# Optimization experiments

Hardware: AMD Instinct MI355X
Metric: run time of the kernel (lower is better)

The kernel has to match this reference:

```python
import jax, jax.numpy as jnp
import numpy as np

N = 100000
E = 1600000
IN, HID, OUT = 128, 32, 32


def gcn_conv(x, ei, ew, W, b, n):
    # PyG GCNConv: symmetric norm with self-loops, edge_attr as edge weight
    h = x @ W                                  # [n, d_out]
    row, col = ei[0], ei[1]
    loop = jnp.arange(n)
    row = jnp.concatenate([row, loop])
    col = jnp.concatenate([col, loop])
    ew = jnp.concatenate([ew, jnp.ones((n,), ew.dtype)])
    deg = jax.ops.segment_sum(ew, col, num_segments=n)
    dinv = jnp.where(deg > 0, jax.lax.rsqrt(deg), 0.0)
    norm = dinv[row] * ew * dinv[col]          # [E+n]
    out = jax.ops.segment_sum(norm[:, None] * h[row], col, num_segments=n)
    return out + b


def setup_inputs() -> dict:
    key = jax.random.key(0)
    ks = jax.random.split(key, 24)
    inp = {}
    for i in range(3):
        inp[f"x{i+1}"] = jax.random.normal(ks[i], (N, IN), jnp.float32)
        inp[f"ei{i+1}"] = jax.random.randint(ks[3 + i], (2, E), 0, N, jnp.int64)
        inp[f"ea{i+1}"] = jax.random.uniform(ks[6 + i], (E,), jnp.float32)
        inp[f"W{i+1}"] = jax.random.normal(ks[9 + i], (IN, HID), jnp.float32) * (IN ** -0.5)
        inp[f"b{i+1}"] = jnp.zeros((HID,), jnp.float32)
        inp[f"Wo{i+1}"] = jax.random.normal(ks[12 + i], (HID, OUT), jnp.float32) * (HID ** -0.5)
        inp[f"bo{i+1}"] = jnp.zeros((OUT,), jnp.float32)
    inp["att_w"] = jax.random.normal(ks[15], (HID, 1), jnp.float32) * (HID ** -0.5)
    return inp


def reference(x1, x2, x3, ei1, ei2, ei3, ea1, ea2, ea3,
              W1, W2, W3, b1, b2, b3,
              Wo1, Wo2, Wo3, bo1, bo2, bo3, att_w):
    xs = [x1, x2, x3]
    eis = [ei1, ei2, ei3]
    eas = [ea1, ea2, ea3]
    Ws = [W1, W2, W3]
    bs = [b1, b2, b3]
    Wos = [Wo1, Wo2, Wo3]
    bos = [bo1, bo2, bo3]

    embs, coefs = [], []
    for x, ei, ea, W, b in zip(xs, eis, eas, Ws, bs):
        e = jax.nn.relu(gcn_conv(x, ei, ea, W, b, N))   # [N, HID]; dropout is eval no-op
        embs.append(e)
        coefs.append(jnp.exp(jax.nn.leaky_relu(e @ att_w)))  # [N, 1]
    coef_sum = coefs[0] + coefs[1] + coefs[2]
    weights = [c / coef_sum for c in coefs]
    h = sum(w * e for w, e in zip(weights, embs))       # [N, HID]

    out = sum(gcn_conv(h, ei, ea, Wo, bo, N)
              for ei, ea, Wo, bo in zip(eis, eas, Wos, bos))
    return (out, weights[0], weights[1], weights[2])
```

## Files before the change

### kernel.cpp

```cpp
#include <hip/hip_runtime.h>
#include <hip/hip_fp16.h>

typedef unsigned short u16;
typedef unsigned int   u32;
typedef _Float16 h2 __attribute__((ext_vector_type(2)));

#define N_NODES 100000
#define N_EDGES 1600000
#define IN_DIM  128
#define HID_DIM 32
#define OUT_DIM 32

#define BK   128
#define NBC  782
#define NBT  (3 * NBC)

#define PB    256
#define BINB  1024
#define CHUNK 18750
#define SC_N  (NBT * PB)
#define SC_CHUNK 2048
#define SC_G  ((SC_N + SC_CHUNK - 1) / SC_CHUNK)
#define CAP  3072
#define GN4  ((N_NODES * 4 + 255) / 256)
#define MM2  ((N_NODES + 63) / 64)

#define KEYB 4
#define NKEY (BK << KEYB)

__device__ inline int ofs_at(const int* __restrict__ rp1, const int* __restrict__ bs, int m) {
    return m ? rp1[m] + bs[(m - 1) >> 11] : 0;
}


__global__ void binhist_kernel(const int* __restrict__ ei0, const int* __restrict__ ei1,
                               const int* __restrict__ ei2, int* __restrict__ hist_t) {
    __shared__ int hloc[NBT];
    for (int i = threadIdx.x; i < NBT; i += blockDim.x) hloc[i] = 0;
    __syncthreads();
    int b = blockIdx.x;
    int beg = b * CHUNK, end = beg + CHUNK;
    for (int e = beg + threadIdx.x; e < end; e += blockDim.x) {
        int c = (e >= 2 * N_EDGES) ? 2 : (e >= N_EDGES ? 1 : 0);
        const int* ei = (c == 0) ? ei0 : (c == 1) ? ei1 : ei2;
        int col = ei[N_EDGES + (e - c * N_EDGES)];
        atomicAdd(&hloc[c * NBC + (col >> 7)], 1);
    }
    __syncthreads();
    for (int g = threadIdx.x; g < NBT; g += blockDim.x)
        hist_t[g * PB + b] = hloc[g];
}


__global__ void scan1_kernel(const int* __restrict__ counts, int* __restrict__ rp1,
                             int* __restrict__ blocksum) {
    __shared__ int wsum[4];
    int tid = threadIdx.x;
    int base = blockIdx.x * SC_CHUNK + tid * 8;
    int vals[8];
    int tsum = 0;
    if (base < SC_N) {
        int4 v0 = *(const int4*)(counts + base);
        int4 v1 = *(const int4*)(counts + base + 4);
        vals[0] = v0.x; vals[1] = v0.y; vals[2] = v0.z; vals[3] = v0.w;
        vals[4] = v1.x; vals[5] = v1.y; vals[6] = v1.z; vals[7] = v1.w;
#pragma unroll
        for (int k = 0; k < 8; k++) tsum += vals[k];
    } else {
#pragma unroll
        for (int k = 0; k < 8; k++) vals[k] = 0;
    }
    int lane = tid & 63, wave = tid >> 6;
    int x = tsum;
    for (int d = 1; d < 64; d <<= 1) {
        int t = __shfl_up(x, d, 64);
        if (lane >= d) x += t;
    }
    if (lane == 63) wsum[wave] = x;
    __syncthreads();
    int woff = 0;
    for (int w = 0; w < wave; w++) woff += wsum[w];
    int run = woff + x - tsum;
    if (base < SC_N) {
#pragma unroll
        for (int k = 0; k < 8; k++) {
            run += vals[k];
            rp1[base + k + 1] = run;
        }
    }
    if (tid == blockDim.x - 1) blocksum[blockIdx.x] = woff + x;
    if (blockIdx.x == 0 && tid == 0) rp1[0] = 0;
}

__global__ void scan2_kernel(int* __restrict__ blocksum, int n) {
    __shared__ int wsum[4];
    int tid = threadIdx.x;
    int lane = tid & 63, wave = tid >> 6;
    int carry = 0;
    for (int base = 0; base < n; base += 256) {
        int i = base + tid;
        int v = (i < n) ? blocksum[i] : 0;
        int x = v;
        for (int d = 1; d < 64; d <<= 1) {
            int t = __shfl_up(x, d, 64);
            if (lane >= d) x += t;
        }
        if (lane == 63) wsum[wave] = x;
        __syncthreads();
        int woff = 0;
        for (int w = 0; w < wave; w++) woff += wsum[w];
        int total = wsum[0] + wsum[1] + wsum[2] + wsum[3];
        if (i < n) blocksum[i] = carry + woff + x - v;
        carry += total;
        __syncthreads();
    }
}


__global__ void binscatter_kernel(const int* __restrict__ ei0, const int* __restrict__ ei1,
                                  const int* __restrict__ ei2,
                                  const float* __restrict__ ea0, const float* __restrict__ ea1,
                                  const float* __restrict__ ea2,
                                  const int* __restrict__ rp1, const int* __restrict__ bsum,
                                  int2* __restrict__ stg) {
    __shared__ int base_l[NBT];
    int b = blockIdx.x;
    for (int g = threadIdx.x; g < NBT; g += blockDim.x)
        base_l[g] = ofs_at(rp1, bsum, g * PB + b);
    __syncthreads();
    int beg = b * CHUNK, end = beg + CHUNK;
    for (int e = beg + threadIdx.x; e < end; e += blockDim.x) {
        int c = (e >= 2 * N_EDGES) ? 2 : (e >= N_EDGES ? 1 : 0);
        int le = e - c * N_EDGES;
        const int* ei = (c == 0) ? ei0 : (c == 1) ? ei1 : ei2;
        const float* ea = (c == 0) ? ea0 : (c == 1) ? ea1 : ea2;
        int row = ei[le];
        int col = ei[N_EDGES + le];
        int g = c * NBC + (col >> 7);
        int slot = atomicAdd(&base_l[g], 1);
        stg[slot] = make_int2(row | ((col & 127) << 17), __float_as_int(ea[le]));
    }
}


__global__ void bucket_sort_kernel(const int2* __restrict__ stg, const int* __restrict__ rp1,
                                   const int* __restrict__ bsum,
                                   u32* __restrict__ csr,
                                   float* __restrict__ dinv, int* __restrict__ row_ptr) {
    __shared__ int2 buf[CAP];
    __shared__ int hist[NKEY];
    __shared__ int fill[NKEY];
    __shared__ float deg[BK];
    __shared__ float dl[BK];
    __shared__ int wsum[4];
    int tid = threadIdx.x;
    int g = blockIdx.x;
    int c = g / NBC;
    int colBase = (g % NBC) << 7;
    for (int i = tid; i < NKEY; i += 256) { hist[i] = 0; fill[i] = 0; }
    if (tid < BK) deg[tid] = 1.0f;
    __syncthreads();
    int beg = ofs_at(rp1, bsum, g * PB);
    int end = (g == NBT - 1) ? 3 * N_EDGES : ofs_at(rp1, bsum, (g + 1) * PB);
    int cnt = end - beg;
    if (cnt > CAP) cnt = CAP;
    for (int i = tid; i < cnt; i += blockDim.x) {
        int2 p = stg[beg + i];
        buf[i] = p;
        int cl = (p.x >> 17) & 127;
        int row = p.x & 0x1FFFF;
        atomicAdd(&hist[(cl << KEYB) | (row >> 13)], 1);
        atomicAdd(&deg[cl], __int_as_float(p.y));
    }
    __syncthreads();
    int base8 = tid * 8;
    int v[8]; int tsum = 0;
#pragma unroll
    for (int k = 0; k < 8; k++) { v[k] = hist[base8 + k]; tsum += v[k]; }
    int lane = tid & 63, wave = tid >> 6;
    int xs = tsum;
    for (int d = 1; d < 64; d <<= 1) {
        int tt = __shfl_up(xs, d, 64);
        if (lane >= d) xs += tt;
    }
    if (lane == 63) wsum[wave] = xs;
    __syncthreads();
    int woff = 0;
    for (int w = 0; w < wave; w++) woff += wsum[w];
    int run = woff + xs - tsum;
#pragma unroll
    for (int k = 0; k < 8; k++) { int t2 = v[k]; hist[base8 + k] = run; run += t2; }
    if (tid < BK) dl[tid] = rsqrtf(deg[tid]);
    __syncthreads();
    for (int i = tid; i < cnt; i += blockDim.x) {
        int2 p = buf[i];
        int cl = (p.x >> 17) & 127;
        int row = p.x & 0x1FFFF;
        int key = (cl << KEYB) | (row >> 13);
        int r = atomicAdd(&fill[key], 1);
        float vv = __int_as_float(p.y) * dl[cl];
        __half h = __float2half(vv);
        u32 hb = (u32)(*(u16*)&h) & 0x7FFF;
        csr[beg + hist[key] + r] = (u32)row | (hb << 17);
    }
    int col = colBase + tid;
    if (tid < BK && col < N_NODES) {
        dinv[(size_t)c * N_NODES + col] = dl[tid];
        row_ptr[(size_t)c * N_NODES + col] = beg + hist[tid << KEYB];
    }
    if (g == NBT - 1 && tid == 0) row_ptr[3 * N_NODES] = 3 * N_EDGES;
}


__device__ inline u32 pack_half2(float a, float b) {
    __half2 h = __floats2half2_rn(a, b);
    union { __half2 h; u32 u; } cv; cv.h = h;
    return cv.u;
}

__device__ inline float2 unpack_half2(u32 u) {
    union { u32 u; __half2 h; } cv; cv.u = u;
    return __half22float2(cv.h);
}

__device__ inline float val15(u32 meta) {
    return unpack_half2(meta >> 17).x;
}

__device__ inline float fdot2h(u32 a, u32 b, float c) {
    union { u32 u; h2 h; } ca, cb; ca.u = a; cb.u = b;
    return __builtin_amdgcn_fdot2(ca.h, cb.h, c, false);
}


__global__ void matmul_in3_kernel(const float* __restrict__ x0, const float* __restrict__ x1,
                                  const float* __restrict__ x2,
                                  const float* __restrict__ W0, const float* __restrict__ W1,
                                  const float* __restrict__ W2,
                                  const float* __restrict__ dinv,
                                  u16* __restrict__ h3) {
    __shared__ u32 Ws2[(IN_DIM / 2) * HID_DIM];
    int c = blockIdx.x / MM2;
    int lb = blockIdx.x % MM2;
    const float* x = (c == 0) ? x0 : (c == 1) ? x1 : x2;
    const float* W = (c == 0) ? W0 : (c == 1) ? W1 : W2;
    for (int i = threadIdx.x; i < (IN_DIM / 2) * HID_DIM; i += blockDim.x) {
        int d = i & 31, jp = i >> 5;
        Ws2[i] = pack_half2(W[(2 * jp) * HID_DIM + d], W[(2 * jp + 1) * HID_DIM + d]);
    }
    __syncthreads();
    int t = threadIdx.x & 7;
    int grp = threadIdx.x >> 3;
    int v0 = lb * 64 + grp * 2;
    if (v0 >= N_NODES) return;
    float a[2][4];
#pragma unroll
    for (int k = 0; k < 2; k++)
#pragma unroll
        for (int d = 0; d < 4; d++) a[k][d] = 0.f;
    const float* xr0 = x + (size_t)v0 * IN_DIM;
    const float* xr1 = xr0 + IN_DIM;
#pragma unroll 4
    for (int q = 0; q < 32; q++) {
        float4 xv0 = *(const float4*)(xr0 + 4 * q);
        float4 xv1 = *(const float4*)(xr1 + 4 * q);
        u32 p00 = pack_half2(xv0.x, xv0.y), p01 = pack_half2(xv0.z, xv0.w);
        u32 p10 = pack_half2(xv1.x, xv1.y), p11 = pack_half2(xv1.z, xv1.w);
        uint4 wA = *(const uint4*)&Ws2[(2 * q) * HID_DIM + 4 * t];
        uint4 wB = *(const uint4*)&Ws2[(2 * q + 1) * HID_DIM + 4 * t];
        a[0][0] = fdot2h(p00, wA.x, a[0][0]); a[0][1] = fdot2h(p00, wA.y, a[0][1]);
        a[0][2] = fdot2h(p00, wA.z, a[0][2]); a[0][3] = fdot2h(p00, wA.w, a[0][3]);
        a[0][0] = fdot2h(p01, wB.x, a[0][0]); a[0][1] = fdot2h(p01, wB.y, a[0][1]);
        a[0][2] = fdot2h(p01, wB.z, a[0][2]); a[0][3] = fdot2h(p01, wB.w, a[0][3]);
        a[1][0] = fdot2h(p10, wA.x, a[1][0]); a[1][1] = fdot2h(p10, wA.y, a[1][1]);
        a[1][2] = fdot2h(p10, wA.z, a[1][2]); a[1][3] = fdot2h(p10, wA.w, a[1][3]);
        a[1][0] = fdot2h(p11, wB.x, a[1][0]); a[1][1] = fdot2h(p11, wB.y, a[1][1]);
        a[1][2] = fdot2h(p11, wB.z, a[1][2]); a[1][3] = fdot2h(p11, wB.w, a[1][3]);
    }
#pragma unroll
    for (int k = 0; k < 2; k++) {
        float s = dinv[(size_t)c * N_NODES + v0 + k];
        uint2 pk = make_uint2(pack_half2(a[k][0] * s, a[k][1] * s),
                              pack_half2(a[k][2] * s, a[k][3] * s));
        *(uint2*)(h3 + ((size_t)c * N_NODES + v0 + k) * HID_DIM + 4 * t) = pk;
    }
}


__global__ void matmul_hid3_kernel(const float* __restrict__ hmix,
                                   const float* __restrict__ Wo0, const float* __restrict__ Wo1,
                                   const float* __restrict__ Wo2,
                                   const float* __restrict__ dinv,
                                   u16* __restrict__ h23) {
    __shared__ u32 Ws2[(HID_DIM / 2) * OUT_DIM];
    int c = blockIdx.x / MM2;
    int lb = blockIdx.x % MM2;
    const float* Wo = (c == 0) ? Wo0 : (c == 1) ? Wo1 : Wo2;
    for (int i = threadIdx.x; i < (HID_DIM / 2) * OUT_DIM; i += blockDim.x) {
        int d = i & 31, jp = i >> 5;
        Ws2[i] = pack_half2(Wo[(2 * jp) * OUT_DIM + d], Wo[(2 * jp + 1) * OUT_DIM + d]);
    }
    __syncthreads();
    int t = threadIdx.x & 7;
    int grp = threadIdx.x >> 3;
    int v0 = lb * 64 + grp * 2;
    if (v0 >= N_NODES) return;
    float a[2][4];
#pragma unroll
    for (int k = 0; k < 2; k++)
#pragma unroll
        for (int d = 0; d < 4; d++) a[k][d] = 0.f;
    const float* hr0 = hmix + (size_t)v0 * HID_DIM;
    const float* hr1 = hr0 + HID_DIM;
#pragma unroll
    for (int q = 0; q < 8; q++) {
        float4 xv0 = *(const float4*)(hr0 + 4 * q);
        float4 xv1 = *(const float4*)(hr1 + 4 * q);
        u32 p00 = pack_half2(xv0.x, xv0.y), p01 = pack_half2(xv0.z, xv0.w);
        u32 p10 = pack_half2(xv1.x, xv1.y), p11 = pack_half2(xv1.z, xv1.w);
        uint4 wA = *(const uint4*)&Ws2[(2 * q) * OUT_DIM + 4 * t];
        uint4 wB = *(const uint4*)&Ws2[(2 * q + 1) * OUT_DIM + 4 * t];
        a[0][0] = fdot2h(p00, wA.x, a[0][0]); a[0][1] = fdot2h(p00, wA.y, a[0][1]);
        a[0][2] = fdot2h(p00, wA.z, a[0][2]); a[0][3] = fdot2h(p00, wA.w, a[0][3]);
        a[0][0] = fdot2h(p01, wB.x, a[0][0]); a[0][1] = fdot2h(p01, wB.y, a[0][1]);
        a[0][2] = fdot2h(p01, wB.z, a[0][2]); a[0][3] = fdot2h(p01, wB.w, a[0][3]);
        a[1][0] = fdot2h(p10, wA.x, a[1][0]); a[1][1] = fdot2h(p10, wA.y, a[1][1]);
        a[1][2] = fdot2h(p10, wA.z, a[1][2]); a[1][3] = fdot2h(p10, wA.w, a[1][3]);
        a[1][0] = fdot2h(p11, wB.x, a[1][0]); a[1][1] = fdot2h(p11, wB.y, a[1][1]);
        a[1][2] = fdot2h(p11, wB.z, a[1][2]); a[1][3] = fdot2h(p11, wB.w, a[1][3]);
    }
#pragma unroll
    for (int k = 0; k < 2; k++) {
        float s = dinv[(size_t)c * N_NODES + v0 + k];
        uint2 pk = make_uint2(pack_half2(a[k][0] * s, a[k][1] * s),
                              pack_half2(a[k][2] * s, a[k][3] * s));
        *(uint2*)(h23 + ((size_t)c * N_NODES + v0 + k) * OUT_DIM + 4 * t) = pk;
    }
}


__global__ void gather_combine_kernel(const int* __restrict__ row_ptr,
                                      const u32* __restrict__ csr,
                                      const u16* __restrict__ h3,
                                      const float* __restrict__ dinv,
                                      const float* __restrict__ b0,
                                      const float* __restrict__ b1,
                                      const float* __restrict__ b2,
                                      const float* __restrict__ att_w,
                                      float* __restrict__ hmix,
                                      float* __restrict__ wout) {
    int gid = blockIdx.x * blockDim.x + threadIdx.x;
    int v = gid >> 2;
    int t = gid & 3;
    if (v >= N_NODES) return;
    float4 wv0 = *(const float4*)(att_w + t * 8);
    float4 wv1 = *(const float4*)(att_w + t * 8 + 4);
    float e[3][8];
    float coef[3];
#pragma unroll
    for (int c = 0; c < 3; c++) {
        const u16* h = h3 + (size_t)c * N_NODES * HID_DIM;
        const float* bb = (c == 0) ? b0 : (c == 1) ? b1 : b2;
        int beg = row_ptr[c * N_NODES + v], end = row_ptr[c * N_NODES + v + 1];
        float a[8];
#pragma unroll
        for (int k = 0; k < 8; k++) a[k] = 0.f;
        int ee = beg;
        for (; ee + 4 <= end; ee += 4) {
            u32 m0 = csr[ee], m1 = csr[ee + 1], m2 = csr[ee + 2], m3 = csr[ee + 3];
            uint4 u0 = *(const uint4*)(h + (size_t)(m0 & 0x1FFFF) * HID_DIM + 8 * t);
            uint4 u1 = *(const uint4*)(h + (size_t)(m1 & 0x1FFFF) * HID_DIM + 8 * t);
            uint4 u2 = *(const uint4*)(h + (size_t)(m2 & 0x1FFFF) * HID_DIM + 8 * t);
            uint4 u3 = *(const uint4*)(h + (size_t)(m3 & 0x1FFFF) * HID_DIM + 8 * t);
            float vl0 = val15(m0), vl1 = val15(m1), vl2 = val15(m2), vl3 = val15(m3);
            float2 f;
            f = unpack_half2(u0.x); a[0] += vl0 * f.x; a[1] += vl0 * f.y;
            f = unpack_half2(u0.y); a[2] += vl0 * f.x; a[3] += vl0 * f.y;
            f = unpack_half2(u0.z); a[4] += vl0 * f.x; a[5] += vl0 * f.y;
            f = unpack_half2(u0.w); a[6] += vl0 * f.x; a[7] += vl0 * f.y;
            f = unpack_half2(u1.x); a[0] += vl1 * f.x; a[1] += vl1 * f.y;
            f = unpack_half2(u1.y); a[2] += vl1 * f.x; a[3] += vl1 * f.y;
            f = unpack_half2(u1.z); a[4] += vl1 * f.x; a[5] += vl1 * f.y;
            f = unpack_half2(u1.w); a[6] += vl1 * f.x; a[7] += vl1 * f.y;
            f = unpack_half2(u2.x); a[0] += vl2 * f.x; a[1] += vl2 * f.y;
            f = unpack_half2(u2.y); a[2] += vl2 * f.x; a[3] += vl2 * f.y;
            f = unpack_half2(u2.z); a[4] += vl2 * f.x; a[5] += vl2 * f.y;
            f = unpack_half2(u2.w); a[6] += vl2 * f.x; a[7] += vl2 * f.y;
            f = unpack_half2(u3.x); a[0] += vl3 * f.x; a[1] += vl3 * f.y;
            f = unpack_half2(u3.y); a[2] += vl3 * f.x; a[3] += vl3 * f.y;
            f = unpack_half2(u3.z); a[4] += vl3 * f.x; a[5] += vl3 * f.y;
            f = unpack_half2(u3.w); a[6] += vl3 * f.x; a[7] += vl3 * f.y;
        }
        for (; ee < end; ee++) {
            u32 m = csr[ee];
            float vl = val15(m);
            uint4 u = *(const uint4*)(h + (size_t)(m & 0x1FFFF) * HID_DIM + 8 * t);
            float2 f;
            f = unpack_half2(u.x); a[0] += vl * f.x; a[1] += vl * f.y;
            f = unpack_half2(u.y); a[2] += vl * f.x; a[3] += vl * f.y;
            f = unpack_half2(u.z); a[4] += vl * f.x; a[5] += vl * f.y;
            f = unpack_half2(u.w); a[6] += vl * f.x; a[7] += vl * f.y;
        }
        float s = dinv[(size_t)c * N_NODES + v];
        uint4 u = *(const uint4*)(h + (size_t)v * HID_DIM + 8 * t);
        float2 f0 = unpack_half2(u.x), f1 = unpack_half2(u.y);
        float2 f2 = unpack_half2(u.z), f3 = unpack_half2(u.w);
        float4 bv0 = *(const float4*)(bb + t * 8);
        float4 bv1 = *(const float4*)(bb + t * 8 + 4);
        e[c][0] = fmaxf(a[0] + s * f0.x + bv0.x, 0.f);
        e[c][1] = fmaxf(a[1] + s * f0.y + bv0.y, 0.f);
        e[c][2] = fmaxf(a[2] + s * f1.x + bv0.z, 0.f);
        e[c][3] = fmaxf(a[3] + s * f1.y + bv0.w, 0.f);
        e[c][4] = fmaxf(a[4] + s * f2.x + bv1.x, 0.f);
        e[c][5] = fmaxf(a[5] + s * f2.y + bv1.y, 0.f);
        e[c][6] = fmaxf(a[6] + s * f3.x + bv1.z, 0.f);
        e[c][7] = fmaxf(a[7] + s * f3.y + bv1.w, 0.f);
        float dot = e[c][0] * wv0.x + e[c][1] * wv0.y + e[c][2] * wv0.z + e[c][3] * wv0.w
                  + e[c][4] * wv1.x + e[c][5] * wv1.y + e[c][6] * wv1.z + e[c][7] * wv1.w;
        dot += __shfl_xor(dot, 1, 64);
        dot += __shfl_xor(dot, 2, 64);
        float lr = (dot > 0.0f) ? dot : 0.01f * dot;
        coef[c] = expf(lr);
    }
    float inv = 1.0f / (coef[0] + coef[1] + coef[2]);
    float w0 = coef[0] * inv, w1 = coef[1] * inv, w2 = coef[2] * inv;
    if (t == 0) {
        wout[v] = w0;
        wout[N_NODES + v] = w1;
        wout[2 * N_NODES + v] = w2;
    }
    float4 r0, r1;
    r0.x = w0 * e[0][0] + w1 * e[1][0] + w2 * e[2][0];
    r0.y = w0 * e[0][1] + w1 * e[1][1] + w2 * e[2][1];
    r0.z = w0 * e[0][2] + w1 * e[1][2] + w2 * e[2][2];
    r0.w = w0 * e[0][3] + w1 * e[1][3] + w2 * e[2][3];
    r1.x = w0 * e[0][4] + w1 * e[1][4] + w2 * e[2][4];
    r1.y = w0 * e[0][5] + w1 * e[1][5] + w2 * e[2][5];
    r1.z = w0 * e[0][6] + w1 * e[1][6] + w2 * e[2][6];
    r1.w = w0 * e[0][7] + w1 * e[1][7] + w2 * e[2][7];
    *(float4*)(hmix + (size_t)v * HID_DIM + t * 8) = r0;
    *(float4*)(hmix + (size_t)v * HID_DIM + t * 8 + 4) = r1;
}


__global__ void gather_out_kernel(const int* __restrict__ row_ptr,
                                  const u32* __restrict__ csr,
                                  const u16* __restrict__ h23,
                                  const float* __restrict__ dinv,
                                  const float* __restrict__ bo0,
                                  const float* __restrict__ bo1,
                                  const float* __restrict__ bo2,
                                  float* __restrict__ out) {
    int gid = blockIdx.x * blockDim.x + threadIdx.x;
    int v = gid >> 2;
    int t = gid & 3;
    if (v >= N_NODES) return;
    float4 p0 = *(const float4*)(bo0 + t * 8);
    float4 p1 = *(const float4*)(bo0 + t * 8 + 4);
    float4 q0 = *(const float4*)(bo1 + t * 8);
    float4 q1 = *(const float4*)(bo1 + t * 8 + 4);
    float4 s0 = *(const float4*)(bo2 + t * 8);
    float4 s1 = *(const float4*)(bo2 + t * 8 + 4);
    float a[8];
    a[0] = p0.x + q0.x + s0.x; a[1] = p0.y + q0.y + s0.y;
    a[2] = p0.z + q0.z + s0.z; a[3] = p0.w + q0.w + s0.w;
    a[4] = p1.x + q1.x + s1.x; a[5] = p1.y + q1.y + s1.y;
    a[6] = p1.z + q1.z + s1.z; a[7] = p1.w + q1.w + s1.w;
#pragma unroll
    for (int c = 0; c < 3; c++) {
        const u16* h2m = h23 + (size_t)c * N_NODES * OUT_DIM;
        int beg = row_ptr[c * N_NODES + v], end = row_ptr[c * N_NODES + v + 1];
        int ee = beg;
        for (; ee + 4 <= end; ee += 4) {
            u32 m0 = csr[ee], m1 = csr[ee + 1], m2 = csr[ee + 2], m3 = csr[ee + 3];
            uint4 u0 = *(const uint4*)(h2m + (size_t)(m0 & 0x1FFFF) * OUT_DIM + 8 * t);
            uint4 u1 = *(const uint4*)(h2m + (size_t)(m1 & 0x1FFFF) * OUT_DIM + 8 * t);
            uint4 u2 = *(const uint4*)(h2m + (size_t)(m2 & 0x1FFFF) * OUT_DIM + 8 * t);
            uint4 u3 = *(const uint4*)(h2m + (size_t)(m3 & 0x1FFFF) * OUT_DIM + 8 * t);
            float vl0 = val15(m0), vl1 = val15(m1), vl2 = val15(m2), vl3 = val15(m3);
            float2 f;
            f = unpack_half2(u0.x); a[0] += vl0 * f.x; a[1] += vl0 * f.y;
            f = unpack_half2(u0.y); a[2] += vl0 * f.x; a[3] += vl0 * f.y;
            f = unpack_half2(u0.z); a[4] += vl0 * f.x; a[5] += vl0 * f.y;
            f = unpack_half2(u0.w); a[6] += vl0 * f.x; a[7] += vl0 * f.y;
            f = unpack_half2(u1.x); a[0] += vl1 * f.x; a[1] += vl1 * f.y;
            f = unpack_half2(u1.y); a[2] += vl1 * f.x; a[3] += vl1 * f.y;
            f = unpack_half2(u1.z); a[4] += vl1 * f.x; a[5] += vl1 * f.y;
            f = unpack_half2(u1.w); a[6] += vl1 * f.x; a[7] += vl1 * f.y;
            f = unpack_half2(u2.x); a[0] += vl2 * f.x; a[1] += vl2 * f.y;
            f = unpack_half2(u2.y); a[2] += vl2 * f.x; a[3] += vl2 * f.y;
            f = unpack_half2(u2.z); a[4] += vl2 * f.x; a[5] += vl2 * f.y;
            f = unpack_half2(u2.w); a[6] += vl2 * f.x; a[7] += vl2 * f.y;
            f = unpack_half2(u3.x); a[0] += vl3 * f.x; a[1] += vl3 * f.y;
            f = unpack_half2(u3.y); a[2] += vl3 * f.x; a[3] += vl3 * f.y;
            f = unpack_half2(u3.z); a[4] += vl3 * f.x; a[5] += vl3 * f.y;
            f = unpack_half2(u3.w); a[6] += vl3 * f.x; a[7] += vl3 * f.y;
        }
        for (; ee < end; ee++) {
            u32 m = csr[ee];
            float vl = val15(m);
            uint4 u = *(const uint4*)(h2m + (size_t)(m & 0x1FFFF) * OUT_DIM + 8 * t);
            float2 f;
            f = unpack_half2(u.x); a[0] += vl * f.x; a[1] += vl * f.y;
            f = unpack_half2(u.y); a[2] += vl * f.x; a[3] += vl * f.y;
            f = unpack_half2(u.z); a[4] += vl * f.x; a[5] += vl * f.y;
            f = unpack_half2(u.w); a[6] += vl * f.x; a[7] += vl * f.y;
        }
        float s = dinv[(size_t)c * N_NODES + v];
        uint4 u = *(const uint4*)(h2m + (size_t)v * OUT_DIM + 8 * t);
        float2 f0 = unpack_half2(u.x), f1 = unpack_half2(u.y);
        float2 f2 = unpack_half2(u.z), f3 = unpack_half2(u.w);
        a[0] += s * f0.x; a[1] += s * f0.y; a[2] += s * f1.x; a[3] += s * f1.y;
        a[4] += s * f2.x; a[5] += s * f2.y; a[6] += s * f3.x; a[7] += s * f3.y;
    }
    float4 o0, o1;
    o0.x = a[0]; o0.y = a[1]; o0.z = a[2]; o0.w = a[3];
    o1.x = a[4]; o1.y = a[5]; o1.z = a[6]; o1.w = a[7];
    *(float4*)(out + (size_t)v * OUT_DIM + t * 8) = o0;
    *(float4*)(out + (size_t)v * OUT_DIM + t * 8 + 4) = o1;
}


extern "C" void kernel_launch(void* const* d_in, const int* in_sizes, int n_in,
                              void* d_out, int out_size, void* d_ws, size_t ws_size,
                              hipStream_t stream) {
    const float* x[3];  const int* ei[3];  const float* ea[3];
    const float* W[3];  const float* b[3]; const float* Wo[3]; const float* bo[3];
    for (int c = 0; c < 3; c++) {
        x[c]  = (const float*)d_in[7 * c + 0];
        ei[c] = (const int*)  d_in[7 * c + 1];
        ea[c] = (const float*)d_in[7 * c + 2];
        W[c]  = (const float*)d_in[7 * c + 3];
        b[c]  = (const float*)d_in[7 * c + 4];
        Wo[c] = (const float*)d_in[7 * c + 5];
        bo[c] = (const float*)d_in[7 * c + 6];
    }
    const float* att_w = (const float*)d_in[21];
    float* out = (float*)d_out;
    float* wout = out + (size_t)N_NODES * OUT_DIM;

    int*   wsb      = (int*)d_ws;
    float* dinv     = (float*)wsb;
    int*   row_ptr  = wsb + 3 * N_NODES;
    int*   blocksum = row_ptr + 3 * N_NODES + 4;
    size_t stg_off  = (size_t)(3 * N_NODES + 3 * N_NODES + 4 + 512);
    stg_off = (stg_off + 3) & ~(size_t)3;
    int2*  stg      = (int2*)(wsb + stg_off);
    u32*   csr      = (u32*)(stg + 3 * (size_t)N_EDGES);
    u16*   hA       = (u16*)(csr + 3 * (size_t)N_EDGES);
    int*   hist_t   = (int*)hA;
    int*   rp1      = hist_t + SC_N;
    float* hmix     = (float*)(hA + 3 * (size_t)N_NODES * HID_DIM);

    const int B = 256;

    binhist_kernel<<<PB, BINB, 0, stream>>>(ei[0], ei[1], ei[2], hist_t);
    scan1_kernel<<<SC_G, B, 0, stream>>>(hist_t, rp1, blocksum);
    scan2_kernel<<<1, B, 0, stream>>>(blocksum, SC_G);
    binscatter_kernel<<<PB, BINB, 0, stream>>>(ei[0], ei[1], ei[2], ea[0], ea[1], ea[2],
                                               rp1, blocksum, stg);
    bucket_sort_kernel<<<NBT, B, 0, stream>>>(stg, rp1, blocksum, csr, dinv, row_ptr);

    matmul_in3_kernel<<<3 * MM2, B, 0, stream>>>(x[0], x[1], x[2], W[0], W[1], W[2],
                                                 dinv, hA);
    gather_combine_kernel<<<GN4, B, 0, stream>>>(row_ptr, csr, hA, dinv,
                                                 b[0], b[1], b[2], att_w, hmix, wout);

    matmul_hid3_kernel<<<3 * MM2, B, 0, stream>>>(hmix, Wo[0], Wo[1], Wo[2], dinv, hA);
    gather_out_kernel<<<GN4, B, 0, stream>>>(row_ptr, csr, hA, dinv,
                                             bo[0], bo[1], bo[2], out);
}
```

Before: 576.8 us.

## Widen sort buckets to 512 columns and drop shared-memory edge staging buffer

Each bucket now covers 512 destination columns instead of 128, so there are 4x fewer bucket-sort blocks, each handling about 8k edges. The shared-memory staging buffer and CAP clamp are removed, and the second pass re-reads the staging array from global memory. Fill counters are replaced by atomically incrementing the scanned histogram in place, and column start offsets are saved separately. This lowers block count and removes the overflow truncation, but each block does more serial work, re-reads global memory and holds a larger 32-entry register array per thread for the scan.

```diff
diff --git a/kernel.cpp b/kernel.cpp
--- a/kernel.cpp
+++ b/kernel.cpp
@@ -11,8 +11,8 @@
 #define HID_DIM 32
 #define OUT_DIM 32
 
-#define BK   128
-#define NBC  782
+#define BK   512
+#define NBC  196
 #define NBT  (3 * NBC)
 
 #define PB    256
@@ -21,7 +21,6 @@
 #define SC_N  (NBT * PB)
 #define SC_CHUNK 2048
 #define SC_G  ((SC_N + SC_CHUNK - 1) / SC_CHUNK)
-#define CAP  3072
 #define GN4  ((N_NODES * 4 + 255) / 256)
 #define MM2  ((N_NODES + 63) / 64)
 
@@ -44,7 +43,7 @@
         int c = (e >= 2 * N_EDGES) ? 2 : (e >= N_EDGES ? 1 : 0);
         const int* ei = (c == 0) ? ei0 : (c == 1) ? ei1 : ei2;
         int col = ei[N_EDGES + (e - c * N_EDGES)];
-        atomicAdd(&hloc[c * NBC + (col >> 7)], 1);
+        atomicAdd(&hloc[c * NBC + (col >> 9)], 1);
     }
     __syncthreads();
     for (int g = threadIdx.x; g < NBT; g += blockDim.x)
@@ -136,9 +135,9 @@
         const float* ea = (c == 0) ? ea0 : (c == 1) ? ea1 : ea2;
         int row = ei[le];
         int col = ei[N_EDGES + le];
-        int g = c * NBC + (col >> 7);
+        int g = c * NBC + (col >> 9);
         int slot = atomicAdd(&base_l[g], 1);
-        stg[slot] = make_int2(row | ((col & 127) << 17), __float_as_int(ea[le]));
+        stg[slot] = make_int2(row | ((col & 511) << 17), __float_as_int(ea[le]));
     }
 }
 
@@ -147,36 +146,34 @@
                                    const int* __restrict__ bsum,
                                    u32* __restrict__ csr,
                                    float* __restrict__ dinv, int* __restrict__ row_ptr) {
-    __shared__ int2 buf[CAP];
     __shared__ int hist[NKEY];
-    __shared__ int fill[NKEY];
+    __shared__ int colStart[BK];
     __shared__ float deg[BK];
     __shared__ float dl[BK];
     __shared__ int wsum[4];
     int tid = threadIdx.x;
     int g = blockIdx.x;
     int c = g / NBC;
-    int colBase = (g % NBC) << 7;
-    for (int i = tid; i < NKEY; i += 256) { hist[i] = 0; fill[i] = 0; }
-    if (tid < BK) deg[tid] = 1.0f;
+    int colBase = (g % NBC) << 9;
+    for (int i = tid; i < NKEY; i += 256) hist[i] = 0;
+    deg[tid] = 1.0f;
+    deg[tid + 256] = 1.0f;
     __syncthreads();
     int beg = ofs_at(rp1, bsum, g * PB);
     int end = (g == NBT - 1) ? 3 * N_EDGES : ofs_at(rp1, bsum, (g + 1) * PB);
     int cnt = end - beg;
-    if (cnt > CAP) cnt = CAP;
     for (int i = tid; i < cnt; i += blockDim.x) {
         int2 p = stg[beg + i];
-        buf[i] = p;
-        int cl = (p.x >> 17) & 127;
+        int cl = (p.x >> 17) & 511;
         int row = p.x & 0x1FFFF;
         atomicAdd(&hist[(cl << KEYB) | (row >> 13)], 1);
         atomicAdd(&deg[cl], __int_as_float(p.y));
     }
     __syncthreads();
-    int base8 = tid * 8;
-    int v[8]; int tsum = 0;
-#pragma unroll
-    for (int k = 0; k < 8; k++) { v[k] = hist[base8 + k]; tsum += v[k]; }
+    int base32 = tid * 32;
+    int v[32]; int tsum = 0;
+#pragma unroll
+    for (int k = 0; k < 32; k++) { v[k] = hist[base32 + k]; tsum += v[k]; }
     int lane = tid & 63, wave = tid >> 6;
     int xs = tsum;
     for (int d = 1; d < 64; d <<= 1) {
@@ -189,24 +186,33 @@
     for (int w = 0; w < wave; w++) woff += wsum[w];
     int run = woff + xs - tsum;
 #pragma unroll
-    for (int k = 0; k < 8; k++) { int t2 = v[k]; hist[base8 + k] = run; run += t2; }
-    if (tid < BK) dl[tid] = rsqrtf(deg[tid]);
+    for (int k = 0; k < 32; k++) {
+        if (k == 0)  colStart[2 * tid]     = run;
+        if (k == 16) colStart[2 * tid + 1] = run;
+        int t2 = v[k]; hist[base32 + k] = run; run += t2;
+    }
+    dl[tid] = rsqrtf(deg[tid]);
+    dl[tid + 256] = rsqrtf(deg[tid + 256]);
     __syncthreads();
     for (int i = tid; i < cnt; i += blockDim.x) {
-        int2 p = buf[i];
-        int cl = (p.x >> 17) & 127;
+        int2 p = stg[beg + i];
+        int cl = (p.x >> 17) & 511;
         int row = p.x & 0x1FFFF;
         int key = (cl << KEYB) | (row >> 13);
-        int r = atomicAdd(&fill[key], 1);
+        int slot = atomicAdd(&hist[key], 1);
         float vv = __int_as_float(p.y) * dl[cl];
         __half h = __float2half(vv);
         u32 hb = (u32)(*(u16*)&h) & 0x7FFF;
-        csr[beg + hist[key] + r] = (u32)row | (hb << 17);
-    }
-    int col = colBase + tid;
-    if (tid < BK && col < N_NODES) {
-        dinv[(size_t)c * N_NODES + col] = dl[tid];
-        row_ptr[(size_t)c * N_NODES + col] = beg + hist[tid << KEYB];
+        csr[beg + slot] = (u32)row | (hb << 17);
+    }
+#pragma unroll
+    for (int q = 0; q < 2; q++) {
+        int cl = tid + q * 256;
+        int col = colBase + cl;
+        if (col < N_NODES) {
+            dinv[(size_t)c * N_NODES + col] = dl[cl];
+            row_ptr[(size_t)c * N_NODES + col] = beg + colStart[cl];
+        }
     }
     if (g == NBT - 1 && tid == 0) row_ptr[3 * N_NODES] = 3 * N_EDGES;
 }
```

Result: faster. 562.5 us (-2.5%).
